# Performance work log

Hardware: AMD Instinct MI355X
Metric: run time of the kernel (lower is better)

## Reference

```python
import jax, jax.numpy as jnp
import numpy as np

THETA = 10.0      # spike threshold
TAU_SR = 1.0      # SRM (psp) kernel time constant
TAU_REF = 1.0     # refractory kernel time constant
SCALE_REF = 2.0   # refractory kernel scale (SLAYER default: -2*theta peak)


@jax.custom_vjp
def spike_fn(v):
    # Heaviside on (membrane - theta); surrogate gradient in bwd (SLAYER-style pdf)
    return (v >= 0.0).astype(v.dtype)

def _spike_fwd(v):
    return spike_fn(v), v

def _spike_bwd(v, g):
    return (g * jnp.exp(-jnp.abs(v) / THETA) / THETA,)

spike_fn.defvjp(_spike_fwd, _spike_bwd)


def alpha_psp(x, tau):
    """Causal conv of x (T, B, F) with alpha kernel eps[k] = (k/tau)*exp(1-k/tau),
    implemented as a 2-state linear recurrence (exact for the discrete kernel)."""
    d = jnp.float32(np.exp(-1.0 / tau))
    c = jnp.float32(np.e / tau)

    def step(carry, xt):
        p, q = carry
        q = d * (q + p)          # q[t] = sum_s x[s]*(t-s)*d^(t-s)
        p = d * p + xt           # p[t] = sum_s x[s]*d^(t-s)
        return (p, q), c * q

    z = jnp.zeros_like(x[0])
    _, out = jax.lax.scan(step, (z, z), x)
    return out


def spike_dyn(u, tau_ref, scale_ref, theta):
    """Threshold-with-refractory dynamics. u: (T, B, F) synaptic drive.
    membrane[t] = u[t] - scale_ref*theta * (alpha refractory conv of past spikes)."""
    d = jnp.float32(np.exp(-1.0 / tau_ref))
    c = jnp.float32(np.e / tau_ref)
    cref = jnp.float32(-scale_ref * theta) * c

    def step(carry, ut):
        p, q = carry
        q = d * (q + p)                       # refractory trace (lag-0 coeff is 0)
        s = spike_fn(ut + cref * q - theta)   # spike if membrane >= theta
        p = d * p + s
        return (p, q), s

    z = jnp.zeros_like(u[0])
    _, s = jax.lax.scan(step, (z, z), u)
    return s


def setup_inputs() -> dict:
    key = jax.random.key(0)
    k1, k2, k3 = jax.random.split(key, 3)
    # sparse binary input spike trains, (B, C, H, W, T) SLAYER layout
    downsampled = (jax.random.uniform(k1, (16, 2, 50, 63, 500)) < 0.1).astype(jnp.float32)
    w1 = jax.random.normal(k2, (1024, 6300), dtype=jnp.float32) * 0.1
    w2 = jax.random.normal(k3, (20, 1024), dtype=jnp.float32) * 0.1
    return {"downsampled": downsampled, "w1": w1, "w2": w2}


def reference(downsampled, w1, w2):
    B, T = downsampled.shape[0], downsampled.shape[-1]
    x = downsampled.reshape(B, -1, T).transpose(2, 0, 1)   # (T, B, 6300)
    p1 = alpha_psp(x, TAU_SR)                              # psp filter
    u1 = jnp.einsum('tbf,of->tbo', p1, w1)                 # fc1 (per-timestep dense)
    s1 = spike_dyn(u1, TAU_REF, SCALE_REF, THETA)          # spike layer 1
    p2 = alpha_psp(s1, TAU_SR)
    u2 = jnp.einsum('tbh,oh->tbo', p2, w2)                 # fc2
    s2 = spike_dyn(u2, TAU_REF, SCALE_REF, THETA)
    return s2.transpose(1, 2, 0)                           # (B, output_size, T)
```

## Files before the change

### kernel.cpp

```cpp
#include <hip/hip_runtime.h>
#include <cstdint>
#include <cstddef>

#define T_N   500
#define B_N   16
#define F_IN  6300
#define KW    198
#define KPAD  6336
#define H1    1024
#define H2    20
#define N2P   32
#define M_N   8000
#define M_PADN 8064

#define DD_C   0.36787944117144233f
#define CC_C   2.718281828459045f
#define THETA_C 10.0f
#define INV2048 4.8828125e-4f

typedef _Float16 half8 __attribute__((ext_vector_type(8)));
typedef __attribute__((ext_vector_type(4))) float f32x4;

__device__ __forceinline__ unsigned short f2h_bits(float x) {
    union { _Float16 h; unsigned short u; } c; c.h = (_Float16)x; return c.u;
}
__device__ __forceinline__ float h2f(unsigned short u) {
    union { _Float16 h; unsigned short u; } c; c.u = u; return (float)c.h;
}

__global__ void prep_fused_k(const float* __restrict__ x,
                             const float* __restrict__ w1,
                             const float* __restrict__ w2,
                             uint32_t* __restrict__ bits_t,
                             unsigned short* __restrict__ w1f,
                             unsigned short* __restrict__ w2f) {
    const int bid = blockIdx.x;
    if (bid < 6336) {
        const int b    = bid & 15;
        const int tmp  = bid >> 4;
        const int w    = tmp % 198;
        const int tch2 = tmp / 198;
        const int t    = tch2 * 256 + threadIdx.x;
        if (t >= 504) return;
        const int m = t * 16 + b;
        uint32_t word = 0u;
        if (t < T_N) {
            const int fbase = w * 32;
            #pragma unroll
            for (int j = 0; j < 32; ++j) {
                const int f = fbase + j;
                float v = 0.f;
                if (f < F_IN) v = x[((size_t)b * F_IN + f) * T_N + t];
                word |= (v != 0.f ? 1u : 0u) << j;
            }
        }
        bits_t[(size_t)w * M_PADN + m] = word;
    } else if (bid < 6336 + 1024) {
        const int o = bid - 6336;
        #pragma unroll 1
        for (int it = 0; it < 25; ++it) {
            const int f = it * 256 + threadIdx.x;
            if (f >= KPAD) break;
            float w = (f < F_IN) ? w1[(size_t)o * F_IN + f] : 0.f;
            const unsigned short h1 = f2h_bits(w);
            const float r1 = w - h2f(h1);
            const unsigned short h2 = f2h_bits(r1 * 2048.0f);
            const size_t base = (size_t)o * KPAD + f;
            w1f[base]                     = h1;
            w1f[(size_t)H1 * KPAD + base] = h2;
        }
    } else {
        const int o = bid - 7360;
        #pragma unroll
        for (int it = 0; it < 4; ++it) {
            const int k = it * 256 + threadIdx.x;
            float w = (o < H2) ? w2[(size_t)o * H1 + k] : 0.f;
            const unsigned short h1 = f2h_bits(w);
            const float r1 = w - h2f(h1);
            const unsigned short h2 = f2h_bits(r1 * 2048.0f);
            const size_t base = (size_t)o * H1 + k;
            w2f[base]                    = h1;
            w2f[(size_t)N2P * H1 + base] = h2;
        }
    }
}

__global__ __launch_bounds__(256, 2)
void gemm1_mfma_k(const uint32_t* __restrict__ bits_t,
                  const unsigned short* __restrict__ w1f,
                  float* __restrict__ u1) {
    __shared__ uint32_t AsU[2][128 * 16];
    __shared__ uint32_t BsU[2][2 * 128 * 16];

    const int tid  = threadIdx.x;
    const int lane = tid & 63;
    const int wave = tid >> 6;
    const int wr = wave >> 1, wc = wave & 1;
    const int n0 = blockIdx.x * 128;
    const int m0 = blockIdx.y * 128;
    const int l15 = lane & 15, g = lane >> 4;

    const unsigned short* bsrc0 =
        w1f + (size_t)(n0 + (lane >> 2)) * KPAD + (lane & 3) * 8;

    const int arow_w = tid & 127;
    const int ah     = tid >> 7;
    const int axor   = (arow_w >> 1) & 3;
    const int apos0  = (2 * ah) ^ axor;
    const int apos1  = (2 * ah + 1) ^ axor;

    f32x4 acc[2][4][4];
    const f32x4 fz = {0.f, 0.f, 0.f, 0.f};
    #pragma unroll
    for (int t = 0; t < 2; ++t)
        #pragma unroll
        for (int i = 0; i < 4; ++i)
            #pragma unroll
            for (int j = 0; j < 4; ++j) acc[t][i][j] = fz;

    int aoff[4], boff[4];
    #pragma unroll
    for (int mi = 0; mi < 4; ++mi) {
        const int ar = wr * 64 + mi * 16 + l15;
        aoff[mi] = ar * 16 + ((g ^ ((ar >> 1) & 3)) << 2);
    }
    #pragma unroll
    for (int ni = 0; ni < 4; ++ni) {
        const int br = wc * 64 + ni * 16 + l15;
        boff[ni] = br * 16 + (g << 2);
    }

#define STAGE_B(tt, bb)                                                        \
    {                                                                          \
        _Pragma("unroll")                                                      \
        for (int j = 0; j < 4; ++j) {                                          \
            const int e    = wave * 4 + j;                                     \
            const int term = e >> 3;                                           \
            const int ii   = e & 7;                                            \
            const unsigned short* src =                                        \
                bsrc0 + (size_t)(term * H1 + ii * 16) * KPAD + (size_t)(tt) * 32; \
            __builtin_amdgcn_global_load_lds(                                  \
                (const __attribute__((address_space(1))) uint32_t*)src,        \
                (__attribute__((address_space(3))) uint32_t*)&BsU[bb][term * 2048 + ii * 256], \
                16, 0, 0);                                                     \
        }                                                                      \
    }

#define UNPACK_A(wrd, bb)                                                      \
    {                                                                          \
        uint32_t v[8];                                                         \
        _Pragma("unroll")                                                      \
        for (int i = 0; i < 8; ++i) {                                          \
            const int b0 = ah * 16 + 2 * i;                                    \
            v[i] = ((((wrd) >> b0) & 1u) ? 0x00003C00u : 0u) |                 \
                   ((((wrd) >> (b0 + 1)) & 1u) ? 0x3C000000u : 0u);            \
        }                                                                      \
        *(uint4*)&AsU[bb][arow_w * 16 + apos0 * 4] = make_uint4(v[0], v[1], v[2], v[3]); \
        *(uint4*)&AsU[bb][arow_w * 16 + apos1 * 4] = make_uint4(v[4], v[5], v[6], v[7]); \
    }

#define COMPUTE(bb)                                                            \
    {                                                                          \
        half8 af[4];                                                           \
        _Pragma("unroll")                                                      \
        for (int mi = 0; mi < 4; ++mi) af[mi] = *(const half8*)&AsU[bb][aoff[mi]]; \
        __builtin_amdgcn_s_setprio(1);                                         \
        _Pragma("unroll")                                                      \
        for (int term = 0; term < 2; ++term) {                                 \
            half8 bfv[4];                                                      \
            _Pragma("unroll")                                                  \
            for (int ni = 0; ni < 4; ++ni)                                     \
                bfv[ni] = *(const half8*)&BsU[bb][term * 2048 + boff[ni]];     \
            _Pragma("unroll")                                                  \
            for (int mi = 0; mi < 4; ++mi)                                     \
                _Pragma("unroll")                                              \
                for (int ni = 0; ni < 4; ++ni)                                 \
                    acc[term][mi][ni] = __builtin_amdgcn_mfma_f32_16x16x32_f16( \
                        af[mi], bfv[ni], acc[term][mi][ni], 0, 0, 0);          \
        }                                                                      \
        __builtin_amdgcn_s_setprio(0);                                         \
    }

#define ITER(tt, curbb)                                                        \
    {                                                                          \
        const uint32_t wnext =                                                 \
            bits_t[(size_t)((tt) + 1) * M_PADN + m0 + arow_w];                 \
        STAGE_B((tt) + 1, (curbb) ^ 1);                                        \
        COMPUTE(curbb);                                                        \
        UNPACK_A(wnext, (curbb) ^ 1);                                          \
        __syncthreads();                                                       \
    }

    {
        const uint32_t w0 = bits_t[(size_t)0 * M_PADN + m0 + arow_w];
        STAGE_B(0, 0);
        UNPACK_A(w0, 0);
    }
    __syncthreads();

    for (int t = 0; t < KW - 2; t += 2) {
        ITER(t, 0);
        ITER(t + 1, 1);
    }
    ITER(KW - 2, 0);
    COMPUTE(1);

#undef ITER
#undef COMPUTE
#undef UNPACK_A
#undef STAGE_B

    #pragma unroll
    for (int mi = 0; mi < 4; ++mi) {
        const int mbase = m0 + wr * 64 + mi * 16 + g * 4;
        #pragma unroll
        for (int ni = 0; ni < 4; ++ni) {
            const int o = n0 + wc * 64 + ni * 16 + l15;
            #pragma unroll
            for (int r = 0; r < 4; ++r)
                u1[(size_t)(mbase + r) * H1 + o] =
                    acc[0][mi][ni][r] + acc[1][mi][ni][r] * INV2048;
        }
    }
}

__global__ void scan1_k(const float* __restrict__ u1, unsigned short* __restrict__ s1f) {
    const int lane = blockIdx.x * 64 + threadIdx.x;
    const float CREF = -20.0f * CC_C;
    float p1 = 0.f, q1 = 0.f, pr = 0.f, qr = 0.f;
    float A[10], Bv[10];

#define STEP1(xv, tidx) {                                   \
        q1 = DD_C * (q1 + p1); p1 = DD_C * p1 + (xv);       \
        const float uu = CC_C * q1;                         \
        qr = DD_C * (qr + pr);                              \
        const float vv = uu + CREF * qr - THETA_C;          \
        const float ss = (vv >= 0.f) ? 1.f : 0.f;           \
        pr = DD_C * pr + ss;                                \
        s1f[(size_t)(tidx) * 16384 + lane] =                \
            (vv >= 0.f) ? (unsigned short)0x3C00 : (unsigned short)0; }

    #pragma unroll
    for (int j = 0; j < 10; ++j) A[j] = u1[(size_t)j * 16384 + lane];
    for (int it = 0; it < 25; ++it) {
        const int gB = 2 * it + 1;
        #pragma unroll
        for (int j = 0; j < 10; ++j) Bv[j] = u1[(size_t)(gB * 10 + j) * 16384 + lane];
        #pragma unroll
        for (int j = 0; j < 10; ++j) STEP1(A[j], (2 * it) * 10 + j);
        if (it < 24) {
            const int gA = 2 * it + 2;
            #pragma unroll
            for (int j = 0; j < 10; ++j) A[j] = u1[(size_t)(gA * 10 + j) * 16384 + lane];
        }
        #pragma unroll
        for (int j = 0; j < 10; ++j) STEP1(Bv[j], gB * 10 + j);
    }
#undef STEP1
}

__global__ __launch_bounds__(256)
void gemm2_mfma_k(const unsigned short* __restrict__ s1f,
                  const unsigned short* __restrict__ w2f,
                  float* __restrict__ u2p) {
    __shared__ uint32_t AsU[128 * 16];
    __shared__ uint32_t BsU[2 * 32 * 16];

    const int tid  = threadIdx.x;
    const int lane = tid & 63;
    const int wave = tid >> 6;
    const int m0 = blockIdx.x * 128;
    const int kc = blockIdx.y;
    const int l15 = lane & 15, g = lane >> 4;

    f32x4 acc[2][2][2];
    const f32x4 fz = {0.f, 0.f, 0.f, 0.f};
    #pragma unroll
    for (int t = 0; t < 2; ++t)
        #pragma unroll
        for (int i = 0; i < 2; ++i)
            #pragma unroll
            for (int j = 0; j < 2; ++j) acc[t][i][j] = fz;

    int aoff[2], boff[2][2];
    #pragma unroll
    for (int mi = 0; mi < 2; ++mi) {
        const int ar = wave * 32 + mi * 16 + l15;
        aoff[mi] = ar * 16 + ((g ^ ((ar >> 1) & 3)) << 2);
    }
    #pragma unroll
    for (int term = 0; term < 2; ++term)
        #pragma unroll
        for (int ni = 0; ni < 2; ++ni) {
            const int br = ni * 16 + l15;
            boff[term][ni] = term * 512 + br * 16 + ((g ^ ((br >> 1) & 3)) << 2);
        }

    for (int kw8 = 0; kw8 < 8; ++kw8) {
        const int kw = kc * 8 + kw8;
        __syncthreads();
        #pragma unroll
        for (int i = 0; i < 2; ++i) {
            const int c   = i * 256 + tid;
            const int row = c >> 2;
            const int kch = c & 3;
            const unsigned short* src =
                s1f + (size_t)(m0 + row) * H1 + kw * 32 + (kch ^ ((row >> 1) & 3)) * 8;
            __builtin_amdgcn_global_load_lds(
                (const __attribute__((address_space(1))) uint32_t*)src,
                (__attribute__((address_space(3))) uint32_t*)&AsU[(i * 256 + wave * 64) * 4],
                16, 0, 0);
        }
        {
            const int c    = tid;
            const int term = c >> 7;
            const int o    = (c >> 2) & 31;
            const int kch  = c & 3;
            const unsigned short* src =
                w2f + (size_t)(term * N2P + o) * H1 + kw * 32 + (kch ^ ((o >> 1) & 3)) * 8;
            __builtin_amdgcn_global_load_lds(
                (const __attribute__((address_space(1))) uint32_t*)src,
                (__attribute__((address_space(3))) uint32_t*)&BsU[wave * 256],
                16, 0, 0);
        }
        __syncthreads();

        half8 af[2];
        #pragma unroll
        for (int mi = 0; mi < 2; ++mi) af[mi] = *(const half8*)&AsU[aoff[mi]];
        #pragma unroll
        for (int term = 0; term < 2; ++term)
            #pragma unroll
            for (int ni = 0; ni < 2; ++ni) {
                const half8 bf = *(const half8*)&BsU[boff[term][ni]];
                #pragma unroll
                for (int mi = 0; mi < 2; ++mi)
                    acc[term][mi][ni] = __builtin_amdgcn_mfma_f32_16x16x32_f16(
                        af[mi], bf, acc[term][mi][ni], 0, 0, 0);
            }
    }

    #pragma unroll
    for (int mi = 0; mi < 2; ++mi) {
        const int mbase = m0 + wave * 32 + mi * 16 + g * 4;
        #pragma unroll
        for (int ni = 0; ni < 2; ++ni) {
            const int o = ni * 16 + l15;
            #pragma unroll
            for (int r = 0; r < 4; ++r)
                u2p[((size_t)kc * M_PADN + mbase + r) * N2P + o] =
                    acc[0][mi][ni][r] + acc[1][mi][ni][r] * INV2048;
        }
    }
}

__global__ void scan2_k(const float* __restrict__ u2p, float* __restrict__ out) {
    const int lane = blockIdx.x * 64 + threadIdx.x;
    if (lane >= 320) return;
    const int b  = lane / 20;
    const int o2 = lane % 20;
    const int boffs = b * N2P + o2;
    const float CREF = -20.0f * CC_C;
    float p1 = 0.f, q1 = 0.f, pr = 0.f, qr = 0.f;
    float A[10], Bv[10];

#define LOAD2(tidx)                                                         \
    (u2p[(size_t)0 * M_PADN * N2P + (size_t)(tidx) * 512 + boffs] +         \
     u2p[(size_t)1 * M_PADN * N2P + (size_t)(tidx) * 512 + boffs] +         \
     u2p[(size_t)2 * M_PADN * N2P + (size_t)(tidx) * 512 + boffs] +         \
     u2p[(size_t)3 * M_PADN * N2P + (size_t)(tidx) * 512 + boffs])

#define STEP2(xv, tidx) {                                   \
        q1 = DD_C * (q1 + p1); p1 = DD_C * p1 + (xv);       \
        const float uu = CC_C * q1;                         \
        qr = DD_C * (qr + pr);                              \
        const float vv = uu + CREF * qr - THETA_C;          \
        const float ss = (vv >= 0.f) ? 1.f : 0.f;           \
        pr = DD_C * pr + ss;                                \
        out[(size_t)lane * T_N + (tidx)] = ss; }

    #pragma unroll
    for (int j = 0; j < 10; ++j) A[j] = LOAD2(j);
    for (int it = 0; it < 25; ++it) {
        const int gB = 2 * it + 1;
        #pragma unroll
        for (int j = 0; j < 10; ++j) Bv[j] = LOAD2(gB * 10 + j);
        #pragma unroll
        for (int j = 0; j < 10; ++j) STEP2(A[j], (2 * it) * 10 + j);
        if (it < 24) {
            const int gA = 2 * it + 2;
            #pragma unroll
            for (int j = 0; j < 10; ++j) A[j] = LOAD2(gA * 10 + j);
        }
        #pragma unroll
        for (int j = 0; j < 10; ++j) STEP2(Bv[j], gB * 10 + j);
    }
#undef STEP2
#undef LOAD2
}

extern "C" void kernel_launch(void* const* d_in, const int* in_sizes, int n_in,
                              void* d_out, int out_size, void* d_ws, size_t ws_size,
                              hipStream_t stream) {
    const float* x  = (const float*)d_in[0];
    const float* w1 = (const float*)d_in[1];
    const float* w2 = (const float*)d_in[2];
    float* out = (float*)d_out;

    char* ws = (char*)d_ws;
    size_t off = 0;
    uint32_t*       bits_t = (uint32_t*)(ws + off);       off += (size_t)KW * M_PADN * 4;
    unsigned short* w1f    = (unsigned short*)(ws + off); off += (size_t)2 * H1 * KPAD * 2;
    unsigned short* w2f    = (unsigned short*)(ws + off); off += (size_t)2 * N2P * H1 * 2;
    float*          u1     = (float*)(ws + off);          off += (size_t)M_PADN * H1 * 4;
    unsigned short* s1f    = (unsigned short*)(ws + off); off += (size_t)M_PADN * H1 * 2;
    float*          u2p    = (float*)(ws + off);          off += (size_t)4 * M_PADN * N2P * 4;
    (void)ws_size; (void)in_sizes; (void)n_in; (void)out_size;

    prep_fused_k  <<<7392,        256, 0, stream>>>(x, w1, w2, bits_t, w1f, w2f);
    gemm1_mfma_k  <<<dim3(8, 63), 256, 0, stream>>>(bits_t, w1f, u1);
    scan1_k       <<<256,         64,  0, stream>>>(u1, s1f);
    gemm2_mfma_k  <<<dim3(63, 4), 256, 0, stream>>>(s1f, w2f, u2p);
    scan2_k       <<<5,           64,  0, stream>>>(u2p, out);
}
```

Before: 358.3 us.

## Expand spike bits to fp16 A fragments in registers, drop A LDS staging

Each wave now loads the packed spike-bit words for its own 16 rows directly from global memory and expands them into fp16 MFMA A operands in registers. This removes the shared-memory A tile, its writes and reads, and frees LDS. The B tile gains an XOR swizzle on the global-to-LDS source offsets and the matching read offsets, meant to reduce LDS bank conflicts. In exchange there are redundant global bit loads across waves and lanes, and more per-iteration VALU work for the bit expansion, which is now repeated by both column waves.

```diff
diff --git a/kernel.cpp b/kernel.cpp
--- a/kernel.cpp
+++ b/kernel.cpp
@@ -89,7 +89,6 @@
 void gemm1_mfma_k(const uint32_t* __restrict__ bits_t,
                   const unsigned short* __restrict__ w1f,
                   float* __restrict__ u1) {
-    __shared__ uint32_t AsU[2][128 * 16];
     __shared__ uint32_t BsU[2][2 * 128 * 16];
 
     const int tid  = threadIdx.x;
@@ -101,13 +100,9 @@
     const int l15 = lane & 15, g = lane >> 4;
 
     const unsigned short* bsrc0 =
-        w1f + (size_t)(n0 + (lane >> 2)) * KPAD + (lane & 3) * 8;
-
-    const int arow_w = tid & 127;
-    const int ah     = tid >> 7;
-    const int axor   = (arow_w >> 1) & 3;
-    const int apos0  = (2 * ah) ^ axor;
-    const int apos1  = (2 * ah + 1) ^ axor;
+        w1f + (size_t)(n0 + (lane >> 2)) * KPAD + ((lane & 3) ^ ((lane >> 3) & 3)) * 8;
+
+    const uint32_t* pbits = bits_t + m0 + wr * 64 + l15;
 
     f32x4 acc[2][4][4];
     const f32x4 fz = {0.f, 0.f, 0.f, 0.f};
@@ -118,16 +113,11 @@
             #pragma unroll
             for (int j = 0; j < 4; ++j) acc[t][i][j] = fz;
 
-    int aoff[4], boff[4];
-    #pragma unroll
-    for (int mi = 0; mi < 4; ++mi) {
-        const int ar = wr * 64 + mi * 16 + l15;
-        aoff[mi] = ar * 16 + ((g ^ ((ar >> 1) & 3)) << 2);
-    }
+    int boff[4];
     #pragma unroll
     for (int ni = 0; ni < 4; ++ni) {
         const int br = wc * 64 + ni * 16 + l15;
-        boff[ni] = br * 16 + (g << 2);
+        boff[ni] = br * 16 + ((g ^ ((br >> 1) & 3)) << 2);
     }
 
 #define STAGE_B(tt, bb)                                                        \
@@ -146,24 +136,27 @@
         }                                                                      \
     }
 
-#define UNPACK_A(wrd, bb)                                                      \
+#define LOAD_W(W, tt)                                                          \
     {                                                                          \
-        uint32_t v[8];                                                         \
         _Pragma("unroll")                                                      \
-        for (int i = 0; i < 8; ++i) {                                          \
-            const int b0 = ah * 16 + 2 * i;                                    \
-            v[i] = ((((wrd) >> b0) & 1u) ? 0x00003C00u : 0u) |                 \
-                   ((((wrd) >> (b0 + 1)) & 1u) ? 0x3C000000u : 0u);            \
-        }                                                                      \
-        *(uint4*)&AsU[bb][arow_w * 16 + apos0 * 4] = make_uint4(v[0], v[1], v[2], v[3]); \
-        *(uint4*)&AsU[bb][arow_w * 16 + apos1 * 4] = make_uint4(v[4], v[5], v[6], v[7]); \
-    }
-
-#define COMPUTE(bb)                                                            \
+        for (int mi = 0; mi < 4; ++mi)                                         \
+            W[mi] = pbits[(size_t)(tt) * M_PADN + mi * 16];                    \
+    }
+
+#define COMPUTE(W, bb)                                                         \
     {                                                                          \
         half8 af[4];                                                           \
         _Pragma("unroll")                                                      \
-        for (int mi = 0; mi < 4; ++mi) af[mi] = *(const half8*)&AsU[bb][aoff[mi]]; \
+        for (int mi = 0; mi < 4; ++mi) {                                       \
+            union { uint32_t u[4]; half8 h; } cv;                              \
+            _Pragma("unroll")                                                  \
+            for (int i = 0; i < 4; ++i) {                                      \
+                const int b0 = g * 8 + 2 * i;                                  \
+                cv.u[i] = (((W[mi] >> b0) & 1u) ? 0x00003C00u : 0u) |          \
+                          (((W[mi] >> (b0 + 1)) & 1u) ? 0x3C000000u : 0u);     \
+            }                                                                  \
+            af[mi] = cv.h;                                                     \
+        }                                                                      \
         __builtin_amdgcn_s_setprio(1);                                         \
         _Pragma("unroll")                                                      \
         for (int term = 0; term < 2; ++term) {                                 \
@@ -181,33 +174,29 @@
         __builtin_amdgcn_s_setprio(0);                                         \
     }
 
-#define ITER(tt, curbb)                                                        \
+#define ITER(tt, cb, WCUR, WNEXT)                                              \
     {                                                                          \
-        const uint32_t wnext =                                                 \
-            bits_t[(size_t)((tt) + 1) * M_PADN + m0 + arow_w];                 \
-        STAGE_B((tt) + 1, (curbb) ^ 1);                                        \
-        COMPUTE(curbb);                                                        \
-        UNPACK_A(wnext, (curbb) ^ 1);                                          \
+        LOAD_W(WNEXT, (tt) + 1);                                               \
+        STAGE_B((tt) + 1, (cb) ^ 1);                                           \
+        COMPUTE(WCUR, cb);                                                     \
         __syncthreads();                                                       \
     }
 
-    {
-        const uint32_t w0 = bits_t[(size_t)0 * M_PADN + m0 + arow_w];
-        STAGE_B(0, 0);
-        UNPACK_A(w0, 0);
-    }
+    uint32_t wA[4], wB[4];
+    LOAD_W(wA, 0);
+    STAGE_B(0, 0);
     __syncthreads();
 
     for (int t = 0; t < KW - 2; t += 2) {
-        ITER(t, 0);
-        ITER(t + 1, 1);
-    }
-    ITER(KW - 2, 0);
-    COMPUTE(1);
+        ITER(t,     0, wA, wB);
+        ITER(t + 1, 1, wB, wA);
+    }
+    ITER(KW - 2, 0, wA, wB);
+    COMPUTE(wB, 1);
 
 #undef ITER
 #undef COMPUTE
-#undef UNPACK_A
+#undef LOAD_W
 #undef STAGE_B
 
     #pragma unroll
```

Result: faster. 349.1 us (-2.6%).
